# Kernel optimization log

Measured on AMD Instinct MI355X. Metric: run time of the kernel, lower is better.

Reference implementation:

```python
import jax, jax.numpy as jnp
from jax import lax
import numpy as np

NUM_CH, LSTM_SIZE, NUM_CLS, SEQ_LEN, NUM_PROPS = 128, 512, 40, 256, 1024

def setup_inputs() -> dict:
    key = jax.random.key(0)
    ks = jax.random.split(key, 16)
    s = 0.05
    H, C = LSTM_SIZE, NUM_CH
    return {
        "data": jax.random.normal(ks[0], (NUM_PROPS, SEQ_LEN, C), jnp.float32),
        "labels": jax.random.randint(ks[1], (NUM_PROPS, 2), 0, NUM_CLS).astype(jnp.int32),
        "proposals": jax.random.uniform(ks[2], (NUM_PROPS, 2), jnp.float32),
        # layer 0 LSTM params (PyTorch gate order i,f,g,o; b = b_ih + b_hh)
        "W_ih_0": jax.random.normal(ks[3], (4 * H, C), jnp.float32) * s,
        "W_hh_0": jax.random.normal(ks[4], (4 * H, H), jnp.float32) * s,
        "b_0": jax.random.normal(ks[5], (4 * H,), jnp.float32) * s,
        # layer 1 LSTM params
        "W_ih_1": jax.random.normal(ks[6], (4 * H, H), jnp.float32) * s,
        "W_hh_1": jax.random.normal(ks[7], (4 * H, H), jnp.float32) * s,
        "b_1": jax.random.normal(ks[8], (4 * H,), jnp.float32) * s,
        # heads
        "W_cls": jax.random.normal(ks[9], (NUM_CLS, H), jnp.float32) * s,
        "b_cls": jnp.zeros((NUM_CLS,), jnp.float32),
        "W_bbox": jax.random.normal(ks[10], (2, H), jnp.float32) * s,
        "b_bbox": jnp.zeros((2,), jnp.float32),
    }

def _lstm_layer(x_tnc, W_ih, W_hh, b):
    # x_tnc: [T, N, C_in]; returns hidden sequence [T, N, H]
    T, N, _ = x_tnc.shape
    H = W_hh.shape[1]
    xg = jnp.einsum('tnc,gc->tng', x_tnc, W_ih) + b  # precompute input projections
    def step(carry, gx):
        h, c = carry
        g = gx + h @ W_hh.T
        i, f, gg, o = jnp.split(g, 4, axis=-1)
        i, f, o = jax.nn.sigmoid(i), jax.nn.sigmoid(f), jax.nn.sigmoid(o)
        c = f * c + i * jnp.tanh(gg)
        h = o * jnp.tanh(c)
        return (h, c), h
    h0 = jnp.zeros((N, H), x_tnc.dtype)
    _, hs = lax.scan(step, (h0, h0), xg)
    return hs

def _forward(data, labels, proposals,
             W_ih_0, W_hh_0, b_0, W_ih_1, W_hh_1, b_1,
             W_cls, b_cls, W_bbox, b_bbox):
    x = jnp.transpose(data, (1, 0, 2))  # [T, N, C]
    x = _lstm_layer(x, W_ih_0, W_hh_0, b_0)
    hs = _lstm_layer(x, W_ih_1, W_hh_1, b_1)
    base_feat = hs[-1]                   # last timestep, [N, H]
    cls_feat = base_feat @ W_cls.T + b_cls
    bbox_feat = base_feat @ W_bbox.T + b_bbox
    # train branch: cross-entropy / loss_div, smooth_l1 * 10
    lbl = labels[:, 0]
    logp = jax.nn.log_softmax(cls_feat, axis=-1)
    cls_loss = -jnp.mean(jnp.take_along_axis(logp, lbl[:, None], axis=1))
    cls_idx = jnp.argmax(cls_feat, axis=1)
    loss_div = 1.0 + jnp.sum((cls_idx == lbl).astype(cls_feat.dtype))
    cls_loss = cls_loss / lax.stop_gradient(loss_div)
    target = proposals / SEQ_LEN
    diff = jnp.abs(bbox_feat - target)
    sl1 = jnp.where(diff < 1.0, 0.5 * diff * diff, diff - 0.5)
    bbox_loss = jnp.mean(sl1) * 10.0
    return jnp.stack([cls_loss, bbox_loss])

def reference(data, labels, proposals,
              W_ih_0, W_hh_0, b_0, W_ih_1, W_hh_1, b_1,
              W_cls, b_cls, W_bbox, b_bbox):
    return _forward(data, labels, proposals,
                    W_ih_0, W_hh_0, b_0, W_ih_1, W_hh_1, b_1,
                    W_cls, b_cls, W_bbox, b_bbox)
```

## Files before the change

### kernel.cpp

```cpp
#include <hip/hip_runtime.h>

typedef unsigned short u16;
typedef __attribute__((ext_vector_type(8))) __bf16 bf16x8;
typedef __attribute__((ext_vector_type(4))) float f32x4;

#define T_SEQ 256
#define N_B   1024
#define C_IN  128
#define H_DIM 512
#define NCLS  40
#define NT0   20
#define NT1   32
#define HSLOT (16*1024*32)

union B8 { bf16x8 v; u16 s[8]; };

__device__ __forceinline__ u16 f32_to_bf16_rne(float x) {
    unsigned u = __float_as_uint(x);
    unsigned rounding = 0x7FFFu + ((u >> 16) & 1u);
    return (u16)((u + rounding) >> 16);
}
__device__ __forceinline__ float bf16_to_f32(u16 h) {
    return __uint_as_float(((unsigned)h) << 16);
}
__device__ __forceinline__ void split2(float x, u16& hi, u16& lo) {
    u16 h = f32_to_bf16_rne(x);
    float hf = bf16_to_f32(h);
    u16 l = f32_to_bf16_rne(x - hf);
    hi = h; lo = l;
}
__device__ __forceinline__ float fast_sigmoid(float x) {
    return 1.0f / (1.0f + __expf(-x));
}
__device__ __forceinline__ float fast_tanh(float x) {
    return 1.0f - 2.0f / (__expf(2.0f * x) + 1.0f);
}

__device__ __forceinline__ void glds16(const void* g, void* l) {
    __builtin_amdgcn_global_load_lds(
        (const __attribute__((address_space(1))) void*)(unsigned long long)(g),
        (__attribute__((address_space(3))) void*)(unsigned int)(unsigned long long)(l),
        16, 0, 0);
}

__global__ void k_pack_w(const float* __restrict__ Wih, const float* __restrict__ Whh,
                         int KX, int NT, u16* __restrict__ hi, u16* __restrict__ lo) {
    size_t idx = (size_t)blockIdx.x * 256 + threadIdx.x;
    size_t total = (size_t)16 * NT * 128 * 32;
    if (idx >= total) return;
    int k = (int)(idx & 31);
    int r = (int)((idx >> 5) & 127);
    int rem = (int)(idx >> 12);
    int kt = rem % NT, ct = rem / NT;
    int gate = r & 3, jl = r >> 2;
    int srow = (gate << 9) + (ct << 5) + jl;
    int kg = (kt << 5) + k;
    float v = (kg < KX) ? Wih[(size_t)srow * KX + kg] : Whh[(size_t)srow * H_DIM + (kg - KX)];
    u16 h, l; split2(v, h, l);
    hi[idx] = h; lo[idx] = l;
}

__device__ __forceinline__ void lstm_tile_body(
    int local_blk,
    const float* __restrict__ Xf32,
    const u16* __restrict__ xAhi, const u16* __restrict__ xAlo, int nxt,
    const u16* __restrict__ hAhi, const u16* __restrict__ hAlo,
    const u16* __restrict__ Whi, const u16* __restrict__ Wlo, int NT,
    const float* __restrict__ bias, float* __restrict__ cbuf,
    u16* __restrict__ oHhi, u16* __restrict__ oHlo, float* __restrict__ oF32,
    char* lds, float* biasT)
{
    int ct = ((blockIdx.x & 7) << 1) | ((local_blk >> 6) & 1);
    int rt = (local_blk >> 3) & 7;
    int n0 = rt << 7;

    int tid  = threadIdx.x;
    int w    = tid >> 6;
    int l    = tid & 63;
    int quad = l >> 4;
    int lr   = l & 15;
    int grp  = w >> 2;
    int wr   = (w & 1) << 6;
    int wc2  = ((w >> 1) & 1) << 6;

    if (tid < 128)
        biasT[tid] = bias[((tid & 3) << 9) + (ct << 5) + (tid >> 2)];

    const size_t wbase = ((size_t)(ct * NT)) << 12;
    bf16x8 sxh[2], sxl[2];

    auto stage_ss = [&](int ss, char* buf) {
        #pragma unroll
        for (int g = 0; g < 2; g++) {
            int kt = (ss << 1) | g;
            char* wavebase = buf + (g << 13) + ((tid >> 6) << 10);
            size_t wo = wbase + ((size_t)kt << 12) + ((size_t)tid << 3);
            glds16(Whi + wo, wavebase + 32768);
            glds16(Wlo + wo, wavebase + 49152);
            if (Xf32 == nullptr || kt >= nxt) {
                const u16 *ph, *pl; int kk;
                if (kt < nxt) { ph = xAhi; pl = xAlo; kk = kt; }
                else          { ph = hAhi; pl = hAlo; kk = kt - nxt; }
                size_t ao = (((size_t)kk * 1024 + n0) << 5) + ((size_t)tid << 3);
                glds16(ph + ao, wavebase);
                glds16(pl + ao, wavebase + 16384);
            }
        }
    };
    auto loadX = [&](int ss) {
        #pragma unroll
        for (int g = 0; g < 2; g++) {
            int kt = (ss << 1) | g;
            int row = tid >> 2, seg = tid & 3;
            const float* p = Xf32 + (size_t)(n0 + row) * 32768 + (kt << 5) + (seg << 3);
            f32x4 x0 = *(const f32x4*)p;
            f32x4 x1 = *(const f32x4*)(p + 4);
            B8 hh, ll;
            #pragma unroll
            for (int e = 0; e < 4; e++) { u16 a, b; split2(x0[e], a, b); hh.s[e] = a; ll.s[e] = b; }
            #pragma unroll
            for (int e = 0; e < 4; e++) { u16 a, b; split2(x1[e], a, b); hh.s[4 + e] = a; ll.s[4 + e] = b; }
            sxh[g] = hh.v; sxl[g] = ll.v;
        }
    };
    auto writeX = [&](char* buf) {
        #pragma unroll
        for (int g = 0; g < 2; g++) {
            char* p = buf + (g << 13) + (tid << 4);
            *(bf16x8*)(p)         = sxh[g];
            *(bf16x8*)(p + 16384) = sxl[g];
        }
    };

    f32x4 acc[4][4];
    #pragma unroll
    for (int i = 0; i < 4; i++)
        #pragma unroll
        for (int j = 0; j < 4; j++)
            acc[i][j] = (f32x4){0.f, 0.f, 0.f, 0.f};

    const int NS = NT >> 1;
    stage_ss(0, lds);
    if (Xf32 != nullptr) { loadX(0); writeX(lds); }
    __syncthreads();

    for (int ss = 0; ss < NS; ss++) {
        char* buf  = lds + ((ss & 1) << 16);
        char* cur  = buf + (grp << 13);
        char* nbuf = lds + (((ss + 1) & 1) << 16);
        bool pf  = (ss + 1 < NS);
        bool pfX = pf && (Xf32 != nullptr) && (((ss + 1) << 1) < nxt);
        if (pf) stage_ss(ss + 1, nbuf);
        if (pfX) loadX(ss + 1);

        bf16x8 ah[4], al[4];
        #pragma unroll
        for (int i = 0; i < 4; i++) {
            int ro = ((wr + (i << 4) + lr) << 6) + (quad << 4);
            ah[i] = *(const bf16x8*)(cur + ro);
            al[i] = *(const bf16x8*)(cur + 16384 + ro);
        }
        #pragma unroll
        for (int jp = 0; jp < 2; jp++) {
            bf16x8 bh[2], bl[2];
            #pragma unroll
            for (int u = 0; u < 2; u++) {
                int j = (jp << 1) | u;
                int ro = ((wc2 + (j << 4) + lr) << 6) + (quad << 4);
                bh[u] = *(const bf16x8*)(cur + 32768 + ro);
                bl[u] = *(const bf16x8*)(cur + 49152 + ro);
            }
            __builtin_amdgcn_s_setprio(1);
            #pragma unroll
            for (int u = 0; u < 2; u++) {
                int j = (jp << 1) | u;
                #pragma unroll
                for (int i = 0; i < 4; i++) {
                    acc[i][j] = __builtin_amdgcn_mfma_f32_16x16x32_bf16(ah[i], bh[u], acc[i][j], 0, 0, 0);
                    acc[i][j] = __builtin_amdgcn_mfma_f32_16x16x32_bf16(al[i], bh[u], acc[i][j], 0, 0, 0);
                    acc[i][j] = __builtin_amdgcn_mfma_f32_16x16x32_bf16(ah[i], bl[u], acc[i][j], 0, 0, 0);
                }
            }
            __builtin_amdgcn_s_setprio(0);
        }

        if (pfX) writeX(nbuf);
        __syncthreads();
    }

    float* G0 = (float*)lds;
    float* G1 = (float*)(lds + 65536);
    {
        float* myG = grp ? G1 : G0;
        #pragma unroll
        for (int i = 0; i < 4; i++)
            #pragma unroll
            for (int j = 0; j < 4; j++)
                #pragma unroll
                for (int r = 0; r < 4; r++) {
                    int rr = wr + (i << 4) + (quad << 2) + r;
                    int col = wc2 + (j << 4) + lr;
                    myG[rr * 128 + (col ^ (((rr >> 2) & 3) << 2))] = acc[i][j][r];
                }
    }
    __syncthreads();

    int jl = tid & 31;
    int rbase = tid >> 5;
    #pragma unroll
    for (int it = 0; it < 8; it++) {
        int row = rbase + (it << 4);
        int cS = (jl << 2) ^ (((row >> 2) & 3) << 2);
        f32x4 g0 = *(const f32x4*)(G0 + row * 128 + cS);
        f32x4 g1 = *(const f32x4*)(G1 + row * 128 + cS);
        float gi = g0[0] + g1[0] + biasT[(jl << 2) + 0];
        float gf = g0[1] + g1[1] + biasT[(jl << 2) + 1];
        float gg = g0[2] + g1[2] + biasT[(jl << 2) + 2];
        float go = g0[3] + g1[3] + biasT[(jl << 2) + 3];
        float si = fast_sigmoid(gi);
        float sf = fast_sigmoid(gf);
        float so = fast_sigmoid(go);
        int n = n0 + row;
        int cidx = (n << 9) + (ct << 5) + jl;
        float cn = sf * cbuf[cidx] + si * fast_tanh(gg);
        cbuf[cidx] = cn;
        float h = so * fast_tanh(cn);
        u16 hh2, hl2; split2(h, hh2, hl2);
        size_t ho = (((size_t)ct * 1024 + n) << 5) + jl;
        oHhi[ho] = hh2; oHlo[ho] = hl2;
        if (oF32) oF32[cidx] = h;
    }
}

__global__ __launch_bounds__(512) void k_lstm_pair(
    int t, const float* __restrict__ data,
    const u16* __restrict__ W0hi, const u16* __restrict__ W0lo,
    const u16* __restrict__ W1hi, const u16* __restrict__ W1lo,
    const float* __restrict__ b0, const float* __restrict__ b1,
    u16* __restrict__ h0hi, u16* __restrict__ h0lo,
    u16* __restrict__ h1hi, u16* __restrict__ h1lo,
    float* __restrict__ c0, float* __restrict__ c1,
    float* __restrict__ bfeat)
{
    __shared__ __align__(16) char lds[131072];
    __shared__ float biasT[128];
    int local_blk = blockIdx.x & 127;

    if (blockIdx.x < 128) {
        if (t == 0) return;
        int s = t - 1;
        const u16* xh = h0hi + (size_t)(s & 1) * HSLOT;
        const u16* xl = h0lo + (size_t)(s & 1) * HSLOT;
        const u16* hh = h1hi + (size_t)((s - 1) & 1) * HSLOT;
        const u16* hl = h1lo + (size_t)((s - 1) & 1) * HSLOT;
        u16* oh = h1hi + (size_t)(s & 1) * HSLOT;
        u16* ol = h1lo + (size_t)(s & 1) * HSLOT;
        lstm_tile_body(local_blk, nullptr, xh, xl, 16, hh, hl,
                       W1hi, W1lo, NT1, b1, c1, oh, ol,
                       (s == T_SEQ - 1) ? bfeat : nullptr, lds, biasT);
    } else {
        if (t >= T_SEQ) return;
        const u16* hh = h0hi + (size_t)((t - 1) & 1) * HSLOT;
        const u16* hl = h0lo + (size_t)((t - 1) & 1) * HSLOT;
        u16* oh = h0hi + (size_t)(t & 1) * HSLOT;
        u16* ol = h0lo + (size_t)(t & 1) * HSLOT;
        lstm_tile_body(local_blk, data + (size_t)t * C_IN, nullptr, nullptr, 4,
                       hh, hl, W0hi, W0lo, NT0, b0, c0, oh, ol,
                       nullptr, lds, biasT);
    }
}

__global__ __launch_bounds__(64) void k_head(
    const float* __restrict__ hfeat, const float* __restrict__ Wcls, const float* __restrict__ bcls,
    const float* __restrict__ Wbb, const float* __restrict__ bbb,
    const int* __restrict__ labels, const float* __restrict__ props,
    float* __restrict__ accum)
{
    __shared__ float hs[H_DIM];
    __shared__ float logits[NCLS];
    __shared__ float bb[2];
    int n = blockIdx.x, t = threadIdx.x;
    for (int k = t; k < H_DIM; k += 64) hs[k] = hfeat[((size_t)n << 9) + k];
    __syncthreads();
    if (t < NCLS) {
        float s = bcls[t];
        const float* w = Wcls + (size_t)t * H_DIM;
        for (int k = 0; k < H_DIM; k++) s += hs[k] * w[k];
        logits[t] = s;
    } else if (t < NCLS + 2) {
        int j = t - NCLS;
        float s = bbb[j];
        const float* w = Wbb + (size_t)j * H_DIM;
        for (int k = 0; k < H_DIM; k++) s += hs[k] * w[k];
        bb[j] = s;
    }
    __syncthreads();
    if (t == 0) {
        float m = logits[0]; int am = 0;
        for (int j = 1; j < NCLS; j++) if (logits[j] > m) { m = logits[j]; am = j; }
        float se = 0.f;
        for (int j = 0; j < NCLS; j++) se += expf(logits[j] - m);
        int lbl = labels[n * 2];
        float logp = logits[lbl] - m - logf(se);
        atomicAdd(&accum[0], -logp);
        if (am == lbl) atomicAdd(&accum[1], 1.0f);
        float s2 = 0.f;
        for (int j = 0; j < 2; j++) {
            float target = props[n * 2 + j] * (1.0f / 256.0f);
            float d = fabsf(bb[j] - target);
            s2 += (d < 1.f) ? 0.5f * d * d : d - 0.5f;
        }
        atomicAdd(&accum[2], s2);
    }
}

__global__ void k_final(const float* __restrict__ accum, float* __restrict__ out) {
    out[0] = (accum[0] * (1.0f / 1024.0f)) / (1.0f + accum[1]);
    out[1] = accum[2] * (10.0f / 2048.0f);
}

extern "C" void kernel_launch(void* const* d_in, const int* in_sizes, int n_in,
                              void* d_out, int out_size, void* d_ws, size_t ws_size,
                              hipStream_t stream) {
    const float* data  = (const float*)d_in[0];
    const int*   labels= (const int*)d_in[1];
    const float* props = (const float*)d_in[2];
    const float* Wih0  = (const float*)d_in[3];
    const float* Whh0  = (const float*)d_in[4];
    const float* b0    = (const float*)d_in[5];
    const float* Wih1  = (const float*)d_in[6];
    const float* Whh1  = (const float*)d_in[7];
    const float* b1    = (const float*)d_in[8];
    const float* Wcls  = (const float*)d_in[9];
    const float* bcls  = (const float*)d_in[10];
    const float* Wbb   = (const float*)d_in[11];
    const float* bbb   = (const float*)d_in[12];
    float* out = (float*)d_out;

    char* ws = (char*)d_ws;
    size_t off = 0;
    auto alloc = [&](size_t bytes) -> void* {
        void* p = ws + off;
        off = (off + bytes + 255) & ~(size_t)255;
        return p;
    };
    const size_t NH = (size_t)N_B * H_DIM;
    const size_t W0E = (size_t)16 * NT0 * 128 * 32;
    const size_t W1E = (size_t)16 * NT1 * 128 * 32;

    u16* W0hi = (u16*)alloc(W0E * 2);
    u16* W0lo = (u16*)alloc(W0E * 2);
    u16* W1hi = (u16*)alloc(W1E * 2);
    u16* W1lo = (u16*)alloc(W1E * 2);
    u16* h0hi = (u16*)alloc(2 * (size_t)HSLOT * 2);
    u16* h0lo = (u16*)alloc(2 * (size_t)HSLOT * 2);
    u16* h1hi = (u16*)alloc(2 * (size_t)HSLOT * 2);
    u16* h1lo = (u16*)alloc(2 * (size_t)HSLOT * 2);
    float* c0   = (float*)alloc(NH * 4);
    float* c1   = (float*)alloc(NH * 4);
    float* bfeat= (float*)alloc(NH * 4);
    float* accum= (float*)alloc(4 * 4);

    k_pack_w<<<(int)(W0E / 256), 256, 0, stream>>>(Wih0, Whh0, C_IN, NT0, W0hi, W0lo);
    k_pack_w<<<(int)(W1E / 256), 256, 0, stream>>>(Wih1, Whh1, H_DIM, NT1, W1hi, W1lo);

    (void)hipMemsetAsync(h0hi + HSLOT, 0, (size_t)HSLOT * 2, stream);
    (void)hipMemsetAsync(h0lo + HSLOT, 0, (size_t)HSLOT * 2, stream);
    (void)hipMemsetAsync(h1hi + HSLOT, 0, (size_t)HSLOT * 2, stream);
    (void)hipMemsetAsync(h1lo + HSLOT, 0, (size_t)HSLOT * 2, stream);
    (void)hipMemsetAsync(c0, 0, NH * 4, stream);
    (void)hipMemsetAsync(c1, 0, NH * 4, stream);
    (void)hipMemsetAsync(accum, 0, 16, stream);

    for (int t = 0; t <= T_SEQ; t++) {
        k_lstm_pair<<<256, 512, 0, stream>>>(
            t, data, W0hi, W0lo, W1hi, W1lo, b0, b1,
            h0hi, h0lo, h1hi, h1lo, c0, c1, bfeat);
    }

    k_head<<<N_B, 64, 0, stream>>>(bfeat, Wcls, bcls, Wbb, bbb, labels, props, accum);
    k_final<<<1, 1, 0, stream>>>(accum, out);
}
```

Before: 7.188 ms.

## Prefetch two stages ahead with explicit vmcnt waits in non-X GEMM path

```diff
diff --git a/kernel.cpp b/kernel.cpp
--- a/kernel.cpp
+++ b/kernel.cpp
@@ -139,20 +139,7 @@
         for (int j = 0; j < 4; j++)
             acc[i][j] = (f32x4){0.f, 0.f, 0.f, 0.f};
 
-    const int NS = NT >> 1;
-    stage_ss(0, lds);
-    if (Xf32 != nullptr) { loadX(0); writeX(lds); }
-    __syncthreads();
-
-    for (int ss = 0; ss < NS; ss++) {
-        char* buf  = lds + ((ss & 1) << 16);
-        char* cur  = buf + (grp << 13);
-        char* nbuf = lds + (((ss + 1) & 1) << 16);
-        bool pf  = (ss + 1 < NS);
-        bool pfX = pf && (Xf32 != nullptr) && (((ss + 1) << 1) < nxt);
-        if (pf) stage_ss(ss + 1, nbuf);
-        if (pfX) loadX(ss + 1);
-
+    auto compute_ss = [&](char* cur) {
         bf16x8 ah[4], al[4];
         #pragma unroll
         for (int i = 0; i < 4; i++) {
@@ -183,9 +170,46 @@
             }
             __builtin_amdgcn_s_setprio(0);
         }
-
-        if (pfX) writeX(nbuf);
+    };
+
+    const int NS = NT >> 1;
+    if (Xf32 != nullptr) {
+        stage_ss(0, lds);
+        loadX(0); writeX(lds);
         __syncthreads();
+        for (int ss = 0; ss < NS; ss++) {
+            char* buf  = lds + ((ss & 1) << 16);
+            char* cur  = buf + (grp << 13);
+            char* nbuf = lds + (((ss + 1) & 1) << 16);
+            bool pf  = (ss + 1 < NS);
+            bool pfX = pf && (((ss + 1) << 1) < nxt);
+            if (pf) stage_ss(ss + 1, nbuf);
+            if (pfX) loadX(ss + 1);
+            compute_ss(cur);
+            if (pfX) writeX(nbuf);
+            __syncthreads();
+        }
+    } else {
+        stage_ss(0, lds);
+        stage_ss(1, lds + 65536);
+        for (int ss = 0; ss < NS; ss++) {
+            char* buf = lds + ((ss & 1) << 16);
+            char* cur = buf + (grp << 13);
+            if (ss + 1 < NS) {
+                asm volatile("s_waitcnt vmcnt(8)" ::: "memory");
+            } else {
+                asm volatile("s_waitcnt vmcnt(0)" ::: "memory");
+            }
+            __builtin_amdgcn_sched_barrier(0);
+            __builtin_amdgcn_s_barrier();
+            __builtin_amdgcn_sched_barrier(0);
+            compute_ss(cur);
+            asm volatile("s_waitcnt lgkmcnt(0)" ::: "memory");
+            __builtin_amdgcn_sched_barrier(0);
+            __builtin_amdgcn_s_barrier();
+            __builtin_amdgcn_sched_barrier(0);
+            if (ss + 2 < NS) stage_ss(ss + 2, buf);
+        }
     }
 
     float* G0 = (float*)lds;
```

New measurement: 7.778 ms. 1.08x slower.
